# Kernel optimization log

Hardware: AMD Instinct MI355X
Metric: run time of the kernel (lower is better)

The kernel has to match this reference:

```python
import jax, jax.numpy as jnp
import numpy as np

DIM = 512
CODEBOOK_SIZE = 8192


def setup_inputs() -> dict:
    key = jax.random.key(0)
    k_x, k_e = jax.random.split(key)
    x = jax.random.normal(k_x, (4, 4096, DIM), dtype=jnp.float32)
    # EuclideanCodebook buffer: embed ~ randn(codebook_size, dim)
    embed = jax.random.normal(k_e, (CODEBOOK_SIZE, DIM), dtype=jnp.float32)
    return {"x": x, "embed": embed}


def reference(x, embed):
    # projection_in / projection_out are Identity (codebook_dim=None)
    shape = x.shape
    flatten = x.reshape(-1, shape[-1])  # [N, D]
    # dist = -(||f||^2 - 2 f @ e^T + ||e||^2)  -> negative squared euclidean
    f_sq = jnp.sum(flatten * flatten, axis=1, keepdims=True)          # [N, 1]
    e_sq = jnp.sum(embed * embed, axis=1)[None, :]                    # [1, K]
    dist = -(f_sq - 2.0 * flatten @ embed.T + e_sq)                   # [N, K]
    embed_ind = jnp.argmax(dist, axis=-1)                             # [N]
    embed_ind = embed_ind.reshape(shape[:-1])                         # [B, S]
    quantize = jnp.take(embed, embed_ind, axis=0)                     # [B, S, D]
    return quantize, embed_ind
```

## Files before the change

### kernel.cpp

```cpp
#include <hip/hip_runtime.h>

#define DIM    512
#define KCODES 8192
#define NROWS  16384
#define NEG_INF -3.402823466e38f
#define MARGIN 2.0f
#define CPR 128

typedef unsigned short ushort_t;
typedef unsigned int uint_t;
typedef __attribute__((ext_vector_type(4))) int   v4i;
typedef __attribute__((ext_vector_type(4))) float v4f;

__device__ inline void dma16(const void* g, void* l) {
    __builtin_amdgcn_global_load_lds(
        (const __attribute__((address_space(1))) unsigned int*)g,
        (__attribute__((address_space(3))) unsigned int*)l, 16, 0, 0);
}

__global__ __launch_bounds__(512) void convert_kernel(
    const float* __restrict__ x, const float* __restrict__ embed,
    int4* __restrict__ e_t8, int4* __restrict__ x_t8,
    float* __restrict__ e_sq, float* __restrict__ esqh,
    float* __restrict__ f_sq,
    float* __restrict__ e_scale, float* __restrict__ f_scale)
{
    __shared__ __align__(16) char buf[32][528];

    const int w = threadIdx.x >> 6;
    const int lane = threadIdx.x & 63;
    const bool isE = blockIdx.x < (KCODES / 32);
    const int rows0 = isE ? blockIdx.x * 32 : (blockIdx.x - KCODES / 32) * 32;
    const float* src_base = isE ? embed : x;

    #pragma unroll
    for (int rr = 0; rr < 4; ++rr) {
        int r_local = w * 4 + rr;
        const float* src = src_base + (size_t)(rows0 + r_local) * DIM + lane * 8;
        float4 a = *(const float4*)src;
        float4 b = *(const float4*)(src + 4);
        float s = a.x*a.x + a.y*a.y + a.z*a.z + a.w*a.w
                + b.x*b.x + b.y*b.y + b.z*b.z + b.w*b.w;
        float am = fmaxf(fmaxf(fmaxf(fabsf(a.x), fabsf(a.y)), fmaxf(fabsf(a.z), fabsf(a.w))),
                         fmaxf(fmaxf(fabsf(b.x), fabsf(b.y)), fmaxf(fabsf(b.z), fabsf(b.w))));
        #pragma unroll
        for (int off = 32; off >= 1; off >>= 1) {
            s += __shfl_xor(s, off, 64);
            am = fmaxf(am, __shfl_xor(am, off, 64));
        }
        float inv = (am > 0.0f) ? 127.0f / am : 0.0f;

        float vq[8] = {a.x, a.y, a.z, a.w, b.x, b.y, b.z, b.w};
        uint_t lo = 0, hi = 0;
        #pragma unroll
        for (int jj = 0; jj < 4; ++jj) {
            lo |= ((uint_t)((int)rintf(vq[jj]     * inv) & 0xff)) << (8 * jj);
            hi |= ((uint_t)((int)rintf(vq[4 + jj] * inv) & 0xff)) << (8 * jj);
        }
        *(int*)&buf[r_local][8 * lane]     = (int)lo;
        *(int*)&buf[r_local][8 * lane + 4] = (int)hi;

        if (lane == 0) {
            int r = rows0 + r_local;
            float sc = am * (1.0f / 127.0f);
            if (isE) { e_sq[r] = s; esqh[r] = -0.5f * s; e_scale[r] = sc; }
            else     { f_sq[r] = s; f_scale[r] = sc; }
        }
    }
    __syncthreads();

    const int t = threadIdx.x;
    #pragma unroll
    for (int i = 0; i < 2; ++i) {
        int idx = t + i * 512;
        int sq  = idx >> 5;
        int row = idx & 31;
        int4 v = *(const int4*)&buf[row][16 * sq];
        if (isE) e_t8[(size_t)sq * KCODES + rows0 + row] = v;
        else     x_t8[(size_t)sq * NROWS  + rows0 + row] = v;
    }
}

__global__ __launch_bounds__(512, 2) void screen_kernel(
    const int4* __restrict__ e_t8, const int4* __restrict__ x_t8,
    const float* __restrict__ esqh,
    const float* __restrict__ e_scale, const float* __restrict__ f_scale,
    float* __restrict__ cand_s, int* __restrict__ cand_i)
{
    __shared__ __align__(16) char EH[2][8][256][16];
    __shared__ __align__(16) char XH[2][8][256][16];

    const int t = threadIdx.x;
    const int w = t >> 6;
    const int lane = t & 63;
    const int quad = lane >> 4;
    const int l15 = lane & 15;
    const int wm = w & 1;
    const int wn = w >> 1;

    const int n = blockIdx.x;
    const int xcd = n & 7;
    const int j = n >> 3;
    const int rt = xcd * 8 + (j & 7);
    const int ct = j >> 3;
    const int row0 = rt * 256;
    const int cbase = ct * 256;

    const bool isE = w < 4;
    const int4* gbase = isE ? (e_t8 + cbase + w * 64 + lane)
                            : (x_t8 + row0 + (w - 4) * 64 + lane);
    const size_t gstride = isE ? KCODES : NROWS;

    v4i acc[8][4];
    #pragma unroll
    for (int mi = 0; mi < 8; ++mi)
        #pragma unroll
        for (int nj = 0; nj < 4; ++nj)
            acc[mi][nj] = (v4i){0, 0, 0, 0};

    auto issue_dma = [&](int S) {
        int buf = S & 1;
        char* ldst = isE ? &EH[buf][0][(w & 3) * 64][0] : &XH[buf][0][(w & 3) * 64][0];
        #pragma unroll
        for (int q = 0; q < 8; ++q) {
            int sq = S * 8 + q;
            dma16(gbase + (size_t)sq * gstride, ldst + q * 256 * 16);
        }
    };

    issue_dma(0);

    for (int S = 0; S < 4; ++S) {
        __syncthreads();
        if (S < 3) issue_dma(S + 1);
        const int buf = S & 1;

        #pragma unroll
        for (int ks = 0; ks < 2; ++ks) {
            const int q = ks * 4 + quad;
            v4i bh[4];
            #pragma unroll
            for (int nj = 0; nj < 4; ++nj)
                bh[nj] = *(const v4i*)(&XH[buf][q][wn * 64 + nj * 16 + l15][0]);
            #pragma unroll
            for (int mi = 0; mi < 8; ++mi) {
                v4i ah = *(const v4i*)(&EH[buf][q][wm * 128 + mi * 16 + l15][0]);
                #pragma unroll
                for (int nj = 0; nj < 4; ++nj)
                    acc[mi][nj] = __builtin_amdgcn_mfma_i32_16x16x64_i8(ah, bh[nj], acc[mi][nj], 0, 0, 0);
            }
        }
    }

    float sfv[4];
    #pragma unroll
    for (int nj = 0; nj < 4; ++nj)
        sfv[nj] = f_scale[row0 + wn * 64 + nj * 16 + l15];

    float b1[4], b2[4];
    int   i1[4], i2[4];
    #pragma unroll
    for (int nj = 0; nj < 4; ++nj) {
        b1[nj] = NEG_INF; b2[nj] = NEG_INF;
        i1[nj] = 0x7fffffff; i2[nj] = 0x7fffffff;
    }

    const float* se_base = e_scale + cbase + wm * 128 + quad * 4;
    const float* eq_base = esqh    + cbase + wm * 128 + quad * 4;

    v4f seC = *(const v4f*)(se_base);
    v4f eqC = *(const v4f*)(eq_base);
    #pragma unroll
    for (int mi = 0; mi < 8; ++mi) {
        v4f seN, eqN;
        if (mi < 7) {
            seN = *(const v4f*)(se_base + (mi + 1) * 16);
            eqN = *(const v4f*)(eq_base + (mi + 1) * 16);
        }
        int cid0 = cbase + wm * 128 + mi * 16 + quad * 4;
        #pragma unroll
        for (int nj = 0; nj < 4; ++nj) {
            #pragma unroll
            for (int jj = 0; jj < 4; ++jj) {
                float sc = fmaf(sfv[nj] * seC[jj], (float)acc[mi][nj][jj], eqC[jj]);
                int cc = cid0 + jj;
                if (sc > b1[nj])      { b2[nj] = b1[nj]; i2[nj] = i1[nj]; b1[nj] = sc; i1[nj] = cc; }
                else if (sc > b2[nj]) { b2[nj] = sc; i2[nj] = cc; }
            }
        }
        seC = seN; eqC = eqN;
    }

    #pragma unroll
    for (int nj = 0; nj < 4; ++nj) {
        float a1 = b1[nj], a2 = b2[nj];
        int   x1 = i1[nj], x2 = i2[nj];
        #pragma unroll
        for (int o = 16; o <= 32; o <<= 1) {
            float c1 = __shfl_xor(a1, o, 64);
            int   j1 = __shfl_xor(x1, o, 64);
            float c2 = __shfl_xor(a2, o, 64);
            int   j2 = __shfl_xor(x2, o, 64);
            if (c1 > a1) {
                a2 = fmaxf(a1, c2); x2 = (a1 >= c2) ? x1 : j2;
                a1 = c1; x1 = j1;
            } else {
                x2 = (a2 >= c1) ? x2 : j1;
                a2 = fmaxf(a2, c1);
            }
        }
        if (quad == 0) {
            int row = row0 + wn * 64 + nj * 16 + l15;
            size_t b = (size_t)row * CPR + (ct * 4 + wm * 2);
            cand_s[b]     = a1;  cand_i[b]     = x1;
            cand_s[b + 1] = a2;  cand_i[b + 1] = x2;
        }
    }
}

__global__ __launch_bounds__(256) void rescore_kernel(
    const float* __restrict__ x, const float* __restrict__ embed,
    const float* __restrict__ e_sq, const float* __restrict__ f_sq,
    const float* __restrict__ cand_s, const int* __restrict__ cand_i,
    float* __restrict__ out)
{
    int row = blockIdx.x * 4 + (threadIdx.x >> 6);
    int lane = threadIdx.x & 63;
    size_t cb = (size_t)row * CPR;

    float cs0 = cand_s[cb + lane];
    float cs1 = cand_s[cb + 64 + lane];
    int   ci0 = cand_i[cb + lane];
    int   ci1 = cand_i[cb + 64 + lane];

    float m = fmaxf(cs0, cs1);
    #pragma unroll
    for (int o = 32; o >= 1; o >>= 1) m = fmaxf(m, __shfl_xor(m, o, 64));

    unsigned long long mask0 = __ballot(cs0 >= m - MARGIN);
    unsigned long long mask1 = __ballot(cs1 >= m - MARGIN);

    const float4* xsrc = (const float4*)(x + (size_t)row * DIM + lane * 8);
    float4 xa = xsrc[0], xb = xsrc[1];
    float fsq = f_sq[row];

    float bd = NEG_INF;
    int   bi = 0x7fffffff;

    #pragma unroll
    for (int s = 0; s < 2; ++s) {
        unsigned long long mask = s ? mask1 : mask0;
        while (mask) {
            int p = __ffsll(mask) - 1;
            mask &= mask - 1;
            int c = __shfl(s ? ci1 : ci0, p);
            const float4* er = (const float4*)(embed + (size_t)c * DIM + lane * 8);
            float4 ea = er[0], eb = er[1];
            float part = xa.x*ea.x + xa.y*ea.y + xa.z*ea.z + xa.w*ea.w
                       + xb.x*eb.x + xb.y*eb.y + xb.z*eb.z + xb.w*eb.w;
            #pragma unroll
            for (int o = 32; o >= 1; o >>= 1) part += __shfl_xor(part, o, 64);
            float d = -((fsq - 2.0f * part) + e_sq[c]);
            if (d > bd || (d == bd && c < bi)) { bd = d; bi = c; }
        }
    }

    const float4* er = (const float4*)(embed + (size_t)bi * DIM + lane * 8);
    float4 qa = er[0], qb = er[1];
    float4* dst = (float4*)(out + (size_t)row * DIM + lane * 8);
    dst[0] = qa; dst[1] = qb;
    if (lane == 0) out[(size_t)NROWS * DIM + row] = (float)bi;
}

extern "C" void kernel_launch(void* const* d_in, const int* in_sizes, int n_in,
                              void* d_out, int out_size, void* d_ws, size_t ws_size,
                              hipStream_t stream)
{
    const float* x     = (const float*)d_in[0];
    const float* embed = (const float*)d_in[1];
    float* out = (float*)d_out;

    float* e_sq    = (float*)d_ws;
    float* esqh    = e_sq + KCODES;
    float* f_sq    = esqh + KCODES;
    float* e_scale = f_sq + NROWS;
    float* f_scale = e_scale + KCODES;
    float* cand_s  = f_scale + NROWS;
    int*   cand_i  = (int*)(cand_s + (size_t)NROWS * CPR);
    int4*  e_t8    = (int4*)(cand_i + (size_t)NROWS * CPR);

    int4* x_t8 = (int4*)d_out;

    (void)in_sizes; (void)n_in; (void)out_size; (void)ws_size;

    convert_kernel<<<(KCODES + NROWS) / 32, 512, 0, stream>>>(
        x, embed, e_t8, x_t8, e_sq, esqh, f_sq, e_scale, f_scale);
    screen_kernel<<<2048, 512, 0, stream>>>(
        e_t8, x_t8, esqh, e_scale, f_scale, cand_s, cand_i);
    rescore_kernel<<<NROWS / 4, 256, 0, stream>>>(
        x, embed, e_sq, f_sq, cand_s, cand_i, out);
}
```

Baseline: 224.6 us.

## Shrink screen tile to 256x128 with 256-thread blocks and finer K pipeline

The int8 screening GEMM tile changes from 256 rows by 256 codes with 8 waves to 256 rows by 128 codes with 4 waves. The grid doubles to 4096 blocks, and the K loop now runs 8 stages of 4 slices each instead of 4 stages of 8. Each wave covers all 128 codes and its own 64 rows, and all waves load both operands. The smaller blocks use less LDS and give finer scheduling granularity. In exchange, the x tile is re-fetched twice as often, and the deeper, shorter pipeline adds more barriers per block. The candidate slot mapping (ct*2) still fills the 128 slots per row.

```diff
diff --git a/kernel.cpp b/kernel.cpp
--- a/kernel.cpp
+++ b/kernel.cpp
@@ -81,22 +81,21 @@
     }
 }
 
-__global__ __launch_bounds__(512, 2) void screen_kernel(
+__global__ __launch_bounds__(256, 2) void screen_kernel(
     const int4* __restrict__ e_t8, const int4* __restrict__ x_t8,
     const float* __restrict__ esqh,
     const float* __restrict__ e_scale, const float* __restrict__ f_scale,
     float* __restrict__ cand_s, int* __restrict__ cand_i)
 {
-    __shared__ __align__(16) char EH[2][8][256][16];
-    __shared__ __align__(16) char XH[2][8][256][16];
+    __shared__ __align__(16) char EH[2][4][128][16];
+    __shared__ __align__(16) char XH[2][4][256][16];
 
     const int t = threadIdx.x;
     const int w = t >> 6;
     const int lane = t & 63;
     const int quad = lane >> 4;
     const int l15 = lane & 15;
-    const int wm = w & 1;
-    const int wn = w >> 1;
+    const int wn = w;
 
     const int n = blockIdx.x;
     const int xcd = n & 7;
@@ -104,12 +103,10 @@
     const int rt = xcd * 8 + (j & 7);
     const int ct = j >> 3;
     const int row0 = rt * 256;
-    const int cbase = ct * 256;
-
-    const bool isE = w < 4;
-    const int4* gbase = isE ? (e_t8 + cbase + w * 64 + lane)
-                            : (x_t8 + row0 + (w - 4) * 64 + lane);
-    const size_t gstride = isE ? KCODES : NROWS;
+    const int cbase = ct * 128;
+
+    const int4* ep = e_t8 + cbase + lane;
+    const int4* xp = x_t8 + row0 + lane;
 
     v4i acc[8][4];
     #pragma unroll
@@ -120,35 +117,31 @@
 
     auto issue_dma = [&](int S) {
         int buf = S & 1;
-        char* ldst = isE ? &EH[buf][0][(w & 3) * 64][0] : &XH[buf][0][(w & 3) * 64][0];
-        #pragma unroll
-        for (int q = 0; q < 8; ++q) {
-            int sq = S * 8 + q;
-            dma16(gbase + (size_t)sq * gstride, ldst + q * 256 * 16);
-        }
+        size_t sq = (size_t)(S * 4 + w);
+        dma16(ep + sq * KCODES,      &EH[buf][w][0][0]);
+        dma16(ep + sq * KCODES + 64, &EH[buf][w][64][0]);
+        #pragma unroll
+        for (int i = 0; i < 4; ++i)
+            dma16(xp + sq * NROWS + i * 64, &XH[buf][w][i * 64][0]);
     };
 
     issue_dma(0);
 
-    for (int S = 0; S < 4; ++S) {
+    for (int S = 0; S < 8; ++S) {
         __syncthreads();
-        if (S < 3) issue_dma(S + 1);
+        if (S < 7) issue_dma(S + 1);
         const int buf = S & 1;
 
-        #pragma unroll
-        for (int ks = 0; ks < 2; ++ks) {
-            const int q = ks * 4 + quad;
-            v4i bh[4];
+        v4i bh[4];
+        #pragma unroll
+        for (int nj = 0; nj < 4; ++nj)
+            bh[nj] = *(const v4i*)(&XH[buf][quad][wn * 64 + nj * 16 + l15][0]);
+        #pragma unroll
+        for (int mi = 0; mi < 8; ++mi) {
+            v4i ah = *(const v4i*)(&EH[buf][quad][mi * 16 + l15][0]);
             #pragma unroll
             for (int nj = 0; nj < 4; ++nj)
-                bh[nj] = *(const v4i*)(&XH[buf][q][wn * 64 + nj * 16 + l15][0]);
-            #pragma unroll
-            for (int mi = 0; mi < 8; ++mi) {
-                v4i ah = *(const v4i*)(&EH[buf][q][wm * 128 + mi * 16 + l15][0]);
-                #pragma unroll
-                for (int nj = 0; nj < 4; ++nj)
-                    acc[mi][nj] = __builtin_amdgcn_mfma_i32_16x16x64_i8(ah, bh[nj], acc[mi][nj], 0, 0, 0);
-            }
+                acc[mi][nj] = __builtin_amdgcn_mfma_i32_16x16x64_i8(ah, bh[nj], acc[mi][nj], 0, 0, 0);
         }
     }
 
@@ -165,8 +158,8 @@
         i1[nj] = 0x7fffffff; i2[nj] = 0x7fffffff;
     }
 
-    const float* se_base = e_scale + cbase + wm * 128 + quad * 4;
-    const float* eq_base = esqh    + cbase + wm * 128 + quad * 4;
+    const float* se_base = e_scale + cbase + quad * 4;
+    const float* eq_base = esqh    + cbase + quad * 4;
 
     v4f seC = *(const v4f*)(se_base);
     v4f eqC = *(const v4f*)(eq_base);
@@ -177,7 +170,7 @@
             seN = *(const v4f*)(se_base + (mi + 1) * 16);
             eqN = *(const v4f*)(eq_base + (mi + 1) * 16);
         }
-        int cid0 = cbase + wm * 128 + mi * 16 + quad * 4;
+        int cid0 = cbase + mi * 16 + quad * 4;
         #pragma unroll
         for (int nj = 0; nj < 4; ++nj) {
             #pragma unroll
@@ -211,7 +204,7 @@
         }
         if (quad == 0) {
             int row = row0 + wn * 64 + nj * 16 + l15;
-            size_t b = (size_t)row * CPR + (ct * 4 + wm * 2);
+            size_t b = (size_t)row * CPR + (size_t)(ct * 2);
             cand_s[b]     = a1;  cand_i[b]     = x1;
             cand_s[b + 1] = a2;  cand_i[b + 1] = x2;
         }
@@ -295,7 +288,7 @@
 
     convert_kernel<<<(KCODES + NROWS) / 32, 512, 0, stream>>>(
         x, embed, e_t8, x_t8, e_sq, esqh, f_sq, e_scale, f_scale);
-    screen_kernel<<<2048, 512, 0, stream>>>(
+    screen_kernel<<<4096, 256, 0, stream>>>(
         e_t8, x_t8, esqh, e_scale, f_scale, cand_s, cand_i);
     rescore_kernel<<<NROWS / 4, 256, 0, stream>>>(
         x, embed, e_sq, f_sq, cand_s, cand_i, out);
```

Result: slower. 249.9 us (+11.3%).
